# Kernel optimization log

Measured on AMD Instinct MI355X. Metric: run time of the kernel, lower is better.

The kernel has to match this reference:

```python
import jax, jax.numpy as jnp
import numpy as np
from jax import lax

SEQ, F, H1, H2, B, WV, OBJ, REL, VOCAB = 33, 20480, 900, 900, 2, 100, 35, 82, 117


def setup_inputs() -> dict:
    key = jax.random.key(0)
    ks = jax.random.split(key, 17)
    s = lambda k, shape: jax.random.normal(k, shape, jnp.float32) * 0.02
    return dict(
        x=jax.random.normal(ks[0], (SEQ, B, F), jnp.float32),
        w_ih1=s(ks[1], (4 * H1, F)), w_hh1=s(ks[2], (4 * H1, H1)),
        b_ih1=s(ks[3], (4 * H1,)), b_hh1=s(ks[4], (4 * H1,)),
        w_ih2=s(ks[5], (SEQ, 4 * H2, H1 + WV)), w_hh2=s(ks[6], (SEQ, 4 * H2, H2)),
        b_ih2=s(ks[7], (SEQ, 4 * H2)), b_hh2=s(ks[8], (SEQ, 4 * H2)),
        w_obj1=s(ks[9], (OBJ, H2)), b_obj1=s(ks[10], (OBJ,)),
        w_rel=s(ks[11], (REL, H2)), b_rel=s(ks[12], (REL,)),
        w_obj2=s(ks[13], (OBJ, H2)), b_obj2=s(ks[14], (OBJ,)),
        embed=s(ks[15], (VOCAB, WV)),
    )


def lstm_cell(xt, h, c, w_ih, w_hh, b_ih, b_hh):
    # torch gate order: input, forget, cell(g), output
    gates = xt @ w_ih.T + h @ w_hh.T + b_ih + b_hh
    i, f, g, o = jnp.split(gates, 4, axis=-1)
    c = jax.nn.sigmoid(f) * c + jax.nn.sigmoid(i) * jnp.tanh(g)
    h = jax.nn.sigmoid(o) * jnp.tanh(c)
    return h, c


def reference(x, w_ih1, w_hh1, b_ih1, b_hh1, w_ih2, w_hh2, b_ih2, b_hh2,
              w_obj1, b_obj1, w_rel, b_rel, w_obj2, b_obj2, embed):
    batch = x.shape[1]
    # layer-1 LSTM over full sequence
    def step1(carry, xt):
        h, c = lstm_cell(xt, carry[0], carry[1], w_ih1, w_hh1, b_ih1, b_hh1)
        return (h, c), h
    h0 = jnp.zeros((batch, H1), x.dtype)
    _, out1 = lax.scan(step1, (h0, h0), x)  # [SEQ, B, H1]

    # layer-2: first SEQ-2 cells with zero word vector, distinct weights per step
    wv0 = jnp.zeros((batch, WV), x.dtype)
    def step2(carry, inp):
        xt, wih, whh, bih, bhh = inp
        h, c = lstm_cell(jnp.concatenate([xt, wv0], axis=1), carry[0], carry[1], wih, whh, bih, bhh)
        return (h, c), None
    h20 = jnp.zeros((batch, H2), x.dtype)
    (h2, c2), _ = lax.scan(step2, (h20, h20),
                           (out1[:SEQ - 2], w_ih2[:SEQ - 2], w_hh2[:SEQ - 2],
                            b_ih2[:SEQ - 2], b_hh2[:SEQ - 2]))

    obj1 = h2 @ w_obj1.T + b_obj1                      # [B, 35]
    wv = embed[jnp.argmax(obj1, axis=1)]               # [B, 100]
    h2, c2 = lstm_cell(jnp.concatenate([out1[SEQ - 2], wv], axis=1), h2, c2,
                       w_ih2[SEQ - 2], w_hh2[SEQ - 2], b_ih2[SEQ - 2], b_hh2[SEQ - 2])

    rel = h2 @ w_rel.T + b_rel                         # [B, 82]
    wv = embed[jnp.argmax(rel, axis=1) + OBJ]
    h2, c2 = lstm_cell(jnp.concatenate([out1[SEQ - 1], wv], axis=1), h2, c2,
                       w_ih2[SEQ - 1], w_hh2[SEQ - 1], b_ih2[SEQ - 1], b_hh2[SEQ - 1])

    obj2 = h2 @ w_obj2.T + b_obj2                      # [B, 35]
    return (obj1, rel, obj2)
```

## Files before the change

kernel.cpp:

```cpp
#include <hip/hip_runtime.h>

#define SEQn 33
#define Fn   20480
#define Hn   900
#define Bn   2
#define WVn  100
#define OBJn 35
#define RELn 82
#define G4n  3600
#define Mn   66
#define NBLK 225

#define KS1  16
#define KSL1 (Fn/KS1)
#define RB1  25
#define RPB1 144
#define NC1  (KSL1/32)
#define WSTR 40
#define THR1 192

typedef __attribute__((ext_vector_type(8))) short bf16x8;
typedef __attribute__((ext_vector_type(4))) float f32x4;

__device__ __forceinline__ float sigf(float v){ return 1.f/(1.f+expf(-v)); }
__device__ __forceinline__ float dot4(float4 a, float4 b){ return a.x*b.x+a.y*b.y+a.z*b.z+a.w*b.w; }
__device__ __forceinline__ float wred(float v){
  #pragma unroll
  for (int d = 32; d >= 1; d >>= 1) v += __shfl_xor(v, d, 64);
  return v;
}
__device__ __forceinline__ float gload(const float* p){
  return __hip_atomic_load((const float*)p, __ATOMIC_RELAXED, __HIP_MEMORY_SCOPE_AGENT);
}
__device__ __forceinline__ void gstore(float* p, float v){
  __hip_atomic_store(p, v, __ATOMIC_RELAXED, __HIP_MEMORY_SCOPE_AGENT);
}
__device__ __forceinline__ unsigned short f2bf(float f){
  unsigned u = __float_as_uint(f);
  unsigned r = u + 0x7FFFu + ((u >> 16) & 1u);
  return (unsigned short)(r >> 16);
}
__device__ __forceinline__ float bf2f(unsigned short h){
  return __uint_as_float(((unsigned)h) << 16);
}

__device__ __forceinline__ void arrive_and_wait(unsigned* bar){
  unsigned g = __hip_atomic_load(&bar[0], __ATOMIC_RELAXED, __HIP_MEMORY_SCOPE_AGENT);
  const unsigned grp = (unsigned)blockIdx.x & 7u;
  const unsigned gsz = (grp == 0u) ? 29u : 28u;
  unsigned c = __hip_atomic_fetch_add(&bar[32 + grp*16], 1u, __ATOMIC_RELAXED, __HIP_MEMORY_SCOPE_AGENT);
  if (c == gsz - 1u) {
    unsigned c2 = __hip_atomic_fetch_add(&bar[16], 1u, __ATOMIC_RELAXED, __HIP_MEMORY_SCOPE_AGENT);
    if (c2 == 7u) {
      __hip_atomic_store(&bar[16], 0u, __ATOMIC_RELAXED, __HIP_MEMORY_SCOPE_AGENT);
      #pragma unroll
      for (int g8 = 0; g8 < 8; ++g8)
        __hip_atomic_store(&bar[32 + g8*16], 0u, __ATOMIC_RELAXED, __HIP_MEMORY_SCOPE_AGENT);
      asm volatile("s_waitcnt vmcnt(0)" ::: "memory");
      __hip_atomic_store(&bar[0], g + 1u, __ATOMIC_RELAXED, __HIP_MEMORY_SCOPE_AGENT);
      return;
    }
  }
  unsigned cur;
  do { __builtin_amdgcn_s_sleep(1);
       cur = __hip_atomic_load(&bar[0], __ATOMIC_RELAXED, __HIP_MEMORY_SCOPE_AGENT);
  } while (cur == g);
}

__device__ __forceinline__ void gbar(unsigned* bar){
  __syncthreads();
  if (threadIdx.x == 0) arrive_and_wait(bar);
  __syncthreads();
}

__device__ __forceinline__ void gbar_lite(unsigned* bar, int wv){
  asm volatile("" ::: "memory");
  if (wv == 0) asm volatile("s_waitcnt vmcnt(0)" ::: "memory");
  __builtin_amdgcn_sched_barrier(0);
  __builtin_amdgcn_s_barrier();
  __builtin_amdgcn_sched_barrier(0);
  if (threadIdx.x == 0) arrive_and_wait(bar);
  __builtin_amdgcn_sched_barrier(0);
  __builtin_amdgcn_s_barrier();
  __builtin_amdgcn_sched_barrier(0);
  asm volatile("" ::: "memory");
}

__global__ __launch_bounds__(THR1) void k1_mfma(
    const float* __restrict__ x, const float* __restrict__ w1,
    float* __restrict__ G1, unsigned* __restrict__ bar)
{
  const int tid = threadIdx.x;
  if (blockIdx.x == 0 && tid < 10) {
    if (tid == 0) __hip_atomic_store(&bar[0], 0u, __ATOMIC_RELAXED, __HIP_MEMORY_SCOPE_AGENT);
    else if (tid == 1) __hip_atomic_store(&bar[16], 0u, __ATOMIC_RELAXED, __HIP_MEMORY_SCOPE_AGENT);
    else __hip_atomic_store(&bar[32 + (tid-2)*16], 0u, __ATOMIC_RELAXED, __HIP_MEMORY_SCOPE_AGENT);
  }
  __shared__ unsigned short WhL[2][RPB1*WSTR], WlL[2][RPB1*WSTR];
  __shared__ unsigned short XhL[2][80*WSTR],  XlL[2][80*WSTR];

  const int rb = blockIdx.x % RB1;
  const int ks = blockIdx.x / RB1;
  const int r0 = rb * RPB1;
  const int kofs = ks * KSL1;
  const int wv_ = tid >> 6;
  const int lane = tid & 63;
  const int p = lane & 15;
  const int q = lane >> 4;

  f32x4 acc[3][5];
  #pragma unroll
  for (int rt = 0; rt < 3; ++rt)
    #pragma unroll
    for (int mt = 0; mt < 5; ++mt) acc[rt][mt] = (f32x4){0.f,0.f,0.f,0.f};

  float4 wr[6], xrg[4];

  #define ISSUE_STAGE(cc)                                                      \
    { const int kbase = kofs + (cc)*32;                                        \
      _Pragma("unroll")                                                        \
      for (int u = 0; u < 6; ++u) {                                            \
        const int idx = tid + u*THR1;                                          \
        const int row = idx >> 3, k4 = idx & 7;                                \
        wr[u] = *(const float4*)(w1 + (size_t)(r0+row)*Fn + kbase + k4*4);     \
      }                                                                        \
      _Pragma("unroll")                                                        \
      for (int u = 0; u < 4; ++u) {                                            \
        const int idx = tid + u*THR1;                                          \
        const int mrow = idx >> 3, k4 = idx & 7;                               \
        xrg[u] = (idx < 640 && mrow < Mn)                                      \
          ? *(const float4*)(x + (size_t)mrow*Fn + kbase + k4*4)               \
          : make_float4(0.f,0.f,0.f,0.f);                                      \
      }                                                                        \
    }

  #define CVTW(dsth, dstl, off, v)                                             \
    { const unsigned short h0=f2bf(v.x), h1=f2bf(v.y), h2=f2bf(v.z), h3=f2bf(v.w); \
      const unsigned short l0=f2bf(v.x-bf2f(h0)), l1=f2bf(v.y-bf2f(h1));       \
      const unsigned short l2=f2bf(v.z-bf2f(h2)), l3=f2bf(v.w-bf2f(h3));       \
      *(uint2*)&dsth[off] = make_uint2((unsigned)h0|((unsigned)h1<<16),        \
                                       (unsigned)h2|((unsigned)h3<<16));       \
      *(uint2*)&dstl[off] = make_uint2((unsigned)l0|((unsigned)l1<<16),        \
                                       (unsigned)l2|((unsigned)l3<<16));       \
    }

  #define WRITE_STAGE(bb)                                                     \
    { _Pragma("unroll")                                                       \
      for (int u = 0; u < 6; ++u) {                                           \
        const int idx = tid + u*THR1;                                         \
        const int row = idx >> 3, k4 = idx & 7;                               \
        CVTW(WhL[bb], WlL[bb], row*WSTR + k4*4, wr[u]);                       \
      }                                                                       \
      _Pragma("unroll")                                                       \
      for (int u = 0; u < 4; ++u) {                                           \
        const int idx = tid + u*THR1;                                         \
        if (idx < 640) {                                                      \
          const int mrow = idx >> 3, k4 = idx & 7;                            \
          CVTW(XhL[bb], XlL[bb], mrow*WSTR + k4*4, xrg[u]);                   \
        }                                                                     \
      }                                                                       \
    }

  ISSUE_STAGE(0);
  WRITE_STAGE(0);
  __syncthreads();

  for (int c = 0; c < NC1; ++c) {
    const int buf = c & 1;
    if (c+1 < NC1) ISSUE_STAGE(c+1);

    bf16x8 Bh[5], Bl[5];
    #pragma unroll
    for (int mt = 0; mt < 5; ++mt) {
      const int moff = (mt*16 + p)*WSTR + q*8;
      Bh[mt] = *(const bf16x8*)&XhL[buf][moff];
      Bl[mt] = *(const bf16x8*)&XlL[buf][moff];
    }
    #pragma unroll
    for (int rt = 0; rt < 3; ++rt) {
      const int roff = ((wv_ + 3*rt)*16 + p)*WSTR + q*8;
      const bf16x8 Ah = *(const bf16x8*)&WhL[buf][roff];
      const bf16x8 Al = *(const bf16x8*)&WlL[buf][roff];
      #pragma unroll
      for (int mt = 0; mt < 5; ++mt) {
        acc[rt][mt] = __builtin_amdgcn_mfma_f32_16x16x32_bf16(Ah, Bh[mt], acc[rt][mt], 0, 0, 0);
        acc[rt][mt] = __builtin_amdgcn_mfma_f32_16x16x32_bf16(Ah, Bl[mt], acc[rt][mt], 0, 0, 0);
        acc[rt][mt] = __builtin_amdgcn_mfma_f32_16x16x32_bf16(Al, Bh[mt], acc[rt][mt], 0, 0, 0);
      }
    }

    if (c+1 < NC1) WRITE_STAGE(buf^1);
    __syncthreads();
  }

  #pragma unroll
  for (int rt = 0; rt < 3; ++rt)
    #pragma unroll
    for (int mt = 0; mt < 5; ++mt) {
      const int m = mt*16 + p;
      if (m < Mn) {
        #pragma unroll
        for (int r4 = 0; r4 < 4; ++r4) {
          const int grow = r0 + (wv_ + 3*rt)*16 + q*4 + r4;
          atomicAdd(&G1[(size_t)grow*Mn + m], acc[rt][mt][r4]);
        }
      }
    }
  #undef ISSUE_STAGE
  #undef WRITE_STAGE
  #undef CVTW
}

__global__ __launch_bounds__(512) void k_rec(
    const float* __restrict__ G1, float* __restrict__ out1, float* __restrict__ h2arr,
    const float* __restrict__ whh1,
    const float* __restrict__ wih2, const float* __restrict__ whh2,
    const float* __restrict__ bih2, const float* __restrict__ bhh2,
    const float* __restrict__ bih1, const float* __restrict__ bhh1,
    const float* __restrict__ wobj1, const float* __restrict__ bobj1,
    const float* __restrict__ wrel,  const float* __restrict__ brel,
    const float* __restrict__ wobj2, const float* __restrict__ bobj2,
    const float* __restrict__ embed, float* __restrict__ dout,
    unsigned* __restrict__ bar)
{
  __shared__ float hls[Bn][904];
  __shared__ float h2l[Bn][904];
  __shared__ float wvls[Bn][104];
  __shared__ float gls[16][68];
  __shared__ float bls[SEQn][16];
  __shared__ float gexA[16][Bn], gexB[16][Bn];
  __shared__ float cA[4][Bn], cB[4][Bn];
  __shared__ float red[4];
  __shared__ int idxls[Bn];

  const int tid = threadIdx.x;
  const int blk = blockIdx.x;
  const int j0 = blk * 4;
  const int wv_ = tid >> 6;
  const int lane = tid & 63;

  if (tid < 8) {
    const int jj = tid >> 1, m = tid & 1;
    cA[jj][m] = 0.f; cB[jj][m] = 0.f;
    gstore(h2arr + ((size_t)0*Bn + m)*Hn + j0 + jj, 0.f);
  }

  for (int qq = tid; qq < 16*Mn; qq += 512) {
    const int rho = qq / Mn, t = qq % Mn;
    const int gate = rho >> 2, jj = rho & 3;
    const size_t rA = (size_t)gate*Hn + j0 + jj;
    gls[rho][t] = G1[rA*Mn + t] + bih1[rA] + bhh1[rA];
  }
  for (int qq = tid; qq < SEQn*16; qq += 512) {
    const int s = qq / 16, rho = qq % 16;
    const int gate = rho >> 2, jj = rho & 3;
    const size_t ro = (size_t)s*G4n + (size_t)gate*Hn + j0 + jj;
    bls[s][rho] = bih2[ro] + bhh2[ro];
  }

  float4 wAreg[2][4];
  #pragma unroll
  for (int ri = 0; ri < 2; ++ri) {
    const int rho = wv_*2 + ri;
    const int gate = rho >> 2, jj = rho & 3;
    const size_t row = (size_t)gate*Hn + j0 + jj;
    #pragma unroll
    for (int e = 0; e < 4; ++e) {
      const int k = lane*4 + e*256;
      wAreg[ri][e] = (k <= Hn-4) ? *(const float4*)(whh1 + row*Hn + k)
                                 : make_float4(0.f,0.f,0.f,0.f);
    }
  }

  float4 wiR[2][4], whR[2][4];
  #define ISSUE_W(sp, KMX)                                                   \
    { _Pragma("unroll")                                                      \
      for (int ri = 0; ri < 2; ++ri) {                                       \
        const int rho = wv_*2 + ri;                                          \
        const int gate = rho >> 2, jj = rho & 3;                             \
        const size_t ro = (size_t)(sp)*G4n + (size_t)gate*Hn + j0 + jj;      \
        const float* wI = wih2 + ro*1000;                                    \
        const float* wH = whh2 + ro*Hn;                                      \
        _Pragma("unroll")                                                    \
        for (int e = 0; e < 4; ++e) {                                        \
          const int k = lane*4 + e*256;                                      \
          if (k <= (KMX)) wiR[ri][e] = *(const float4*)(wI + k);             \
          if (k <= 896)   whR[ri][e] = *(const float4*)(wH + k);             \
        }                                                                    \
      }                                                                      \
    }

  #define UPD_A(ivar)                                                        \
    { const float cc = sigf(gexA[4+jj][m])*cA[jj][m]                         \
                     + sigf(gexA[jj][m])*tanhf(gexA[8+jj][m]);               \
      cA[jj][m] = cc;                                                        \
      gstore(out1 + ((size_t)(ivar)*Bn + m)*Hn + j0 + jj,                    \
             sigf(gexA[12+jj][m])*tanhf(cc)); }

  #define UPD_B(svar)                                                        \
    { const float cc = sigf(gexB[4+jj][m])*cB[jj][m]                         \
                     + sigf(gexB[jj][m])*tanhf(gexB[8+jj][m]);               \
      cB[jj][m] = cc;                                                        \
      gstore(h2arr + ((size_t)((svar)+1)*Bn + m)*Hn + j0 + jj,               \
             sigf(gexB[12+jj][m])*tanhf(cc)); }

  ISSUE_W(0, 896);
  __syncthreads();

  if (lane == 0) {
    #pragma unroll
    for (int ri = 0; ri < 2; ++ri) {
      const int rho = wv_*2 + ri;
      gexA[rho][0] = gls[rho][0];
      gexA[rho][1] = gls[rho][1];
    }
  }
  __syncthreads();
  if (tid < 8) { const int jj = tid >> 1, m = tid & 1; UPD_A(0); }
  gbar(bar);

  for (int iv = 1; iv <= 31; ++iv) {
    const int s = iv - 1;
    float4 hv[2][4], h2v[2][4];
    #pragma unroll
    for (int e = 0; e < 4; ++e) {
      const int k = lane*4 + e*256;
      #pragma unroll
      for (int m = 0; m < 2; ++m) {
        hv[m][e]  = (k <= 896) ? *(const float4*)(out1  + ((size_t)s*Bn + m)*Hn + k)
                               : make_float4(0.f,0.f,0.f,0.f);
        h2v[m][e] = (k <= 896) ? *(const float4*)(h2arr + ((size_t)s*Bn + m)*Hn + k)
                               : make_float4(0.f,0.f,0.f,0.f);
      }
    }
    #pragma unroll
    for (int ri = 0; ri < 2; ++ri) {
      const int rho = wv_*2 + ri;
      float a0=0.f, a1=0.f, b0=0.f, b1=0.f;
      #pragma unroll
      for (int e = 0; e < 4; ++e) {
        const int k = lane*4 + e*256;
        if (k <= 896) {
          a0 += dot4(wAreg[ri][e], hv[0][e]);  a1 += dot4(wAreg[ri][e], hv[1][e]);
          b0 += dot4(wiR[ri][e],   hv[0][e]);  b1 += dot4(wiR[ri][e],   hv[1][e]);
          b0 += dot4(whR[ri][e],  h2v[0][e]);  b1 += dot4(whR[ri][e],  h2v[1][e]);
        }
      }
      a0 = wred(a0); a1 = wred(a1); b0 = wred(b0); b1 = wred(b1);
      if (lane == 0) {
        gexA[rho][0] = a0 + gls[rho][iv*Bn + 0];
        gexA[rho][1] = a1 + gls[rho][iv*Bn + 1];
        const float bb = bls[s][rho];
        gexB[rho][0] = b0 + bb;
        gexB[rho][1] = b1 + bb;
      }
    }
    asm volatile("s_waitcnt lgkmcnt(0)" ::: "memory");
    __builtin_amdgcn_sched_barrier(0);
    ISSUE_W(iv, (iv >= 31) ? 996 : 896);
    __builtin_amdgcn_sched_barrier(0);
    __builtin_amdgcn_s_barrier();
    __builtin_amdgcn_sched_barrier(0);
    if (tid < 8) {
      const int jj = tid >> 1, m = tid & 1;
      UPD_A(iv);
      UPD_B(s);
    }
    gbar_lite(bar, wv_);
  }

  for (int i = 32; i < 37; ++i) {
    if (i == 33 || i == 35) {
      if (wv_ < 2) {
        const int m = wv_;
        const int nout = (i == 33) ? OBJn : RELn;
        const int off = (i == 33) ? 0 : Bn*OBJn;
        float v = -1e30f; int idx = 0;
        for (int o = lane; o < nout; o += 64) {
          float t = gload(dout + off + m*nout + o);
          if (t > v) { v = t; idx = o; }
        }
        #pragma unroll
        for (int d = 32; d >= 1; d >>= 1) {
          float ov = __shfl_xor(v, d, 64);
          int   oi = __shfl_xor(idx, d, 64);
          if (ov > v || (ov == v && oi < idx)) { v = ov; idx = oi; }
        }
        if (lane == 0) idxls[m] = idx + ((i == 35) ? OBJn : 0);
      }
      __syncthreads();
      for (int qq = tid; qq < Bn*104; qq += 512) {
        const int m = qq / 104, v4 = qq % 104;
        wvls[m][v4] = (v4 < WVn) ? embed[(size_t)idxls[m]*WVn + v4] : 0.f;
      }
      __syncthreads();
    }

    const bool hasA = (i == 32);
    const int  s = (i == 33) ? 31 : (i == 35) ? 32 : -1;
    const bool hasB = (s >= 0);
    const int  srcA = (i == 35) ? 32 : i-1;

    if (hasA || i == 35) {
      for (int qq = tid; qq < 1808; qq += 512) {
        const int m = qq / 904, kk = qq % 904;
        hls[m][kk] = (kk < 900)
          ? gload(out1 + ((size_t)srcA*Bn + m)*Hn + kk) : 0.f;
      }
    }
    if (hasB) {
      for (int qq = tid; qq < 1808; qq += 512) {
        const int m = qq / 904, kk = qq % 904;
        h2l[m][kk] = (kk < 900)
          ? gload(h2arr + ((size_t)s*Bn + m)*Hn + kk) : 0.f;
      }
    }
    __syncthreads();

    if (hasA) {
      #pragma unroll
      for (int ri = 0; ri < 2; ++ri) {
        const int rho = wv_*2 + ri;
        float a0 = 0.f, a1 = 0.f;
        #pragma unroll
        for (int e = 0; e < 4; ++e) {
          const int k = lane*4 + e*256;
          if (k <= Hn-4) {
            a0 += dot4(wAreg[ri][e], *(const float4*)&hls[0][k]);
            a1 += dot4(wAreg[ri][e], *(const float4*)&hls[1][k]);
          }
        }
        a0 = wred(a0); a1 = wred(a1);
        if (lane == 0) {
          gexA[rho][0] = a0 + gls[rho][32*Bn + 0];
          gexA[rho][1] = a1 + gls[rho][32*Bn + 1];
        }
      }
    }

    if (hasB) {
      #pragma unroll
      for (int ri = 0; ri < 2; ++ri) {
        const int rho = wv_*2 + ri;
        float b0 = 0.f, b1 = 0.f;
        #pragma unroll
        for (int e = 0; e < 4; ++e) {
          const int k = lane*4 + e*256;
          if (k <= 896) {
            b0 += dot4(wiR[ri][e], *(const float4*)&hls[0][k]);
            b1 += dot4(wiR[ri][e], *(const float4*)&hls[1][k]);
            b0 += dot4(whR[ri][e], *(const float4*)&h2l[0][k]);
            b1 += dot4(whR[ri][e], *(const float4*)&h2l[1][k]);
          } else if (k >= 900 && k <= 996) {
            b0 += dot4(wiR[ri][e], *(const float4*)&wvls[0][k-900]);
            b1 += dot4(wiR[ri][e], *(const float4*)&wvls[1][k-900]);
          }
        }
        b0 = wred(b0); b1 = wred(b1);
        if (lane == 0) {
          const float bb = bls[s][rho];
          gexB[rho][0] = b0 + bb;
          gexB[rho][1] = b1 + bb;
        }
      }
      if (i == 33) ISSUE_W(32, 996);
    }

    if (i == 32 || i == 34 || i == 36) {
      const int nout = (i == 34) ? RELn : OBJn;
      const float* wh  = (i == 32) ? wobj1 : (i == 34) ? wrel : wobj2;
      const float* bh_ = (i == 32) ? bobj1 : (i == 34) ? brel : bobj2;
      const int off = (i == 32) ? 0 : (i == 34) ? (Bn*OBJn) : (Bn*OBJn + Bn*RELn);
      const int hb = (i == 32) ? 31 : (i == 34) ? 32 : 33;
      if (blk < nout*Bn) {
        const int o = blk >> 1, m = blk & 1;
        float p = 0.f;
        if (tid < 225) {
          const float4 wv4 = *(const float4*)(wh + (size_t)o*Hn + tid*4);
          const float* hp = h2arr + ((size_t)hb*Bn + m)*Hn + tid*4;
          p = wv4.x*gload(hp+0) + wv4.y*gload(hp+1)
            + wv4.z*gload(hp+2) + wv4.w*gload(hp+3);
        }
        if (wv_ < 4) {
          const float pr = wred(p);
          if (lane == 0) red[wv_] = pr;
        }
        __syncthreads();
        if (tid == 0)
          gstore(&dout[off + m*nout + o], red[0]+red[1]+red[2]+red[3] + bh_[o]);
      }
    }

    __syncthreads();
    if (tid < 8) {
      const int jj = tid >> 1, m = tid & 1;
      if (hasA) UPD_A(32);
      if (i == 33) UPD_B(31);
      if (i == 35) UPD_B(32);
    }

    if (i < 36) gbar(bar);
  }
  #undef ISSUE_W
  #undef UPD_A
  #undef UPD_B
}

extern "C" void kernel_launch(void* const* d_in, const int* in_sizes, int n_in,
                              void* d_out, int out_size, void* d_ws, size_t ws_size,
                              hipStream_t stream)
{
  (void)in_sizes; (void)n_in; (void)out_size; (void)ws_size;
  const float* x     = (const float*)d_in[0];
  const float* wih1  = (const float*)d_in[1];
  const float* whh1  = (const float*)d_in[2];
  const float* bih1  = (const float*)d_in[3];
  const float* bhh1  = (const float*)d_in[4];
  const float* wih2  = (const float*)d_in[5];
  const float* whh2  = (const float*)d_in[6];
  const float* bih2  = (const float*)d_in[7];
  const float* bhh2  = (const float*)d_in[8];
  const float* wobj1 = (const float*)d_in[9];
  const float* bobj1 = (const float*)d_in[10];
  const float* wrel  = (const float*)d_in[11];
  const float* brel  = (const float*)d_in[12];
  const float* wobj2 = (const float*)d_in[13];
  const float* bobj2 = (const float*)d_in[14];
  const float* embed = (const float*)d_in[15];
  float* dout = (float*)d_out;

  float* ws = (float*)d_ws;
  float* G1    = ws;
  float* out1  = G1 + (size_t)G4n*Mn;
  float* h2arr = out1 + (size_t)SEQn*Bn*Hn;
  unsigned* bar = (unsigned*)(h2arr + (size_t)34*Bn*Hn);

  hipMemsetAsync(G1, 0, (size_t)G4n*Mn*sizeof(float), stream);
  hipLaunchKernelGGL(k1_mfma, dim3(RB1*KS1), dim3(THR1), 0, stream, x, wih1, G1, bar);

  void* args[19];
  args[0]  = (void*)&G1;    args[1]  = (void*)&out1;  args[2]  = (void*)&h2arr;
  args[3]  = (void*)&whh1;  args[4]  = (void*)&wih2;  args[5]  = (void*)&whh2;
  args[6]  = (void*)&bih2;  args[7]  = (void*)&bhh2;  args[8]  = (void*)&bih1;
  args[9]  = (void*)&bhh1;  args[10] = (void*)&wobj1; args[11] = (void*)&bobj1;
  args[12] = (void*)&wrel;  args[13] = (void*)&brel;  args[14] = (void*)&wobj2;
  args[15] = (void*)&bobj2; args[16] = (void*)&embed; args[17] = (void*)&dout;
  args[18] = (void*)&bar;
  hipLaunchCooperativeKernel((void*)k_rec, dim3(NBLK), dim3(512), args, 0, stream);
}
```

Measured before the change: 475.7 us.

## Split recurrent kernel over twice the blocks and double-buffer per-step weight prefetch

The recurrent cooperative kernel now runs 450 blocks of 256 threads, each owning 2 hidden units instead of 4. The grid barrier is widened to 16 arrival groups to match. Layer-2 step weights are kept in two register buffers, so the next step's weights are loaded before the current step's dot products rather than after. This aims to hide weight-load latency and spread the per-step work across more CUs. The kernel is also launched with an ordinary launch instead of a cooperative one, which relies on all 450 blocks being co-resident and adds barrier arrivals and register pressure.

```diff
diff --git a/kernel.cpp b/kernel.cpp
--- a/kernel.cpp
+++ b/kernel.cpp
@@ -9,7 +9,7 @@
 #define RELn 82
 #define G4n  3600
 #define Mn   66
-#define NBLK 225
+#define NBLK 450
 
 #define KS1  16
 #define KSL1 (Fn/KS1)
@@ -46,16 +46,16 @@
 
 __device__ __forceinline__ void arrive_and_wait(unsigned* bar){
   unsigned g = __hip_atomic_load(&bar[0], __ATOMIC_RELAXED, __HIP_MEMORY_SCOPE_AGENT);
-  const unsigned grp = (unsigned)blockIdx.x & 7u;
-  const unsigned gsz = (grp == 0u) ? 29u : 28u;
+  const unsigned grp = (unsigned)blockIdx.x & 15u;
+  const unsigned gsz = (grp < 2u) ? 29u : 28u;
   unsigned c = __hip_atomic_fetch_add(&bar[32 + grp*16], 1u, __ATOMIC_RELAXED, __HIP_MEMORY_SCOPE_AGENT);
   if (c == gsz - 1u) {
     unsigned c2 = __hip_atomic_fetch_add(&bar[16], 1u, __ATOMIC_RELAXED, __HIP_MEMORY_SCOPE_AGENT);
-    if (c2 == 7u) {
+    if (c2 == 15u) {
       __hip_atomic_store(&bar[16], 0u, __ATOMIC_RELAXED, __HIP_MEMORY_SCOPE_AGENT);
       #pragma unroll
-      for (int g8 = 0; g8 < 8; ++g8)
-        __hip_atomic_store(&bar[32 + g8*16], 0u, __ATOMIC_RELAXED, __HIP_MEMORY_SCOPE_AGENT);
+      for (int g16 = 0; g16 < 16; ++g16)
+        __hip_atomic_store(&bar[32 + g16*16], 0u, __ATOMIC_RELAXED, __HIP_MEMORY_SCOPE_AGENT);
       asm volatile("s_waitcnt vmcnt(0)" ::: "memory");
       __hip_atomic_store(&bar[0], g + 1u, __ATOMIC_RELAXED, __HIP_MEMORY_SCOPE_AGENT);
       return;
@@ -91,7 +91,7 @@
     float* __restrict__ G1, unsigned* __restrict__ bar)
 {
   const int tid = threadIdx.x;
-  if (blockIdx.x == 0 && tid < 10) {
+  if (blockIdx.x == 0 && tid < 18) {
     if (tid == 0) __hip_atomic_store(&bar[0], 0u, __ATOMIC_RELAXED, __HIP_MEMORY_SCOPE_AGENT);
     else if (tid == 1) __hip_atomic_store(&bar[16], 0u, __ATOMIC_RELAXED, __HIP_MEMORY_SCOPE_AGENT);
     else __hip_atomic_store(&bar[32 + (tid-2)*16], 0u, __ATOMIC_RELAXED, __HIP_MEMORY_SCOPE_AGENT);
@@ -211,7 +211,7 @@
   #undef CVTW
 }
 
-__global__ __launch_bounds__(512) void k_rec(
+__global__ __launch_bounds__(256, 2) void k_rec(
     const float* __restrict__ G1, float* __restrict__ out1, float* __restrict__ h2arr,
     const float* __restrict__ whh1,
     const float* __restrict__ wih2, const float* __restrict__ whh2,
@@ -226,34 +226,34 @@
   __shared__ float hls[Bn][904];
   __shared__ float h2l[Bn][904];
   __shared__ float wvls[Bn][104];
-  __shared__ float gls[16][68];
-  __shared__ float bls[SEQn][16];
-  __shared__ float gexA[16][Bn], gexB[16][Bn];
-  __shared__ float cA[4][Bn], cB[4][Bn];
+  __shared__ float gls[8][68];
+  __shared__ float bls[SEQn][8];
+  __shared__ float gexA[8][Bn], gexB[8][Bn];
+  __shared__ float cA[2][Bn], cB[2][Bn];
   __shared__ float red[4];
   __shared__ int idxls[Bn];
 
   const int tid = threadIdx.x;
   const int blk = blockIdx.x;
-  const int j0 = blk * 4;
+  const int j0 = blk * 2;
   const int wv_ = tid >> 6;
   const int lane = tid & 63;
 
-  if (tid < 8) {
+  if (tid < 4) {
     const int jj = tid >> 1, m = tid & 1;
     cA[jj][m] = 0.f; cB[jj][m] = 0.f;
     gstore(h2arr + ((size_t)0*Bn + m)*Hn + j0 + jj, 0.f);
   }
 
-  for (int qq = tid; qq < 16*Mn; qq += 512) {
+  for (int qq = tid; qq < 8*Mn; qq += 256) {
     const int rho = qq / Mn, t = qq % Mn;
-    const int gate = rho >> 2, jj = rho & 3;
+    const int gate = rho >> 1, jj = rho & 1;
     const size_t rA = (size_t)gate*Hn + j0 + jj;
     gls[rho][t] = G1[rA*Mn + t] + bih1[rA] + bhh1[rA];
   }
-  for (int qq = tid; qq < SEQn*16; qq += 512) {
-    const int s = qq / 16, rho = qq % 16;
-    const int gate = rho >> 2, jj = rho & 3;
+  for (int qq = tid; qq < SEQn*8; qq += 256) {
+    const int s = qq / 8, rho = qq % 8;
+    const int gate = rho >> 1, jj = rho & 1;
     const size_t ro = (size_t)s*G4n + (size_t)gate*Hn + j0 + jj;
     bls[s][rho] = bih2[ro] + bhh2[ro];
   }
@@ -262,7 +262,7 @@
   #pragma unroll
   for (int ri = 0; ri < 2; ++ri) {
     const int rho = wv_*2 + ri;
-    const int gate = rho >> 2, jj = rho & 3;
+    const int gate = rho >> 1, jj = rho & 1;
     const size_t row = (size_t)gate*Hn + j0 + jj;
     #pragma unroll
     for (int e = 0; e < 4; ++e) {
@@ -272,39 +272,89 @@
     }
   }
 
-  float4 wiR[2][4], whR[2][4];
-  #define ISSUE_W(sp, KMX)                                                   \
+  float4 wiR0[2][4], whR0[2][4], wiR1[2][4], whR1[2][4];
+  #define ISSUE_W(sp, WI, WH, KMX)                                           \
     { _Pragma("unroll")                                                      \
       for (int ri = 0; ri < 2; ++ri) {                                       \
         const int rho = wv_*2 + ri;                                          \
-        const int gate = rho >> 2, jj = rho & 3;                             \
+        const int gate = rho >> 1, jj = rho & 1;                             \
         const size_t ro = (size_t)(sp)*G4n + (size_t)gate*Hn + j0 + jj;      \
         const float* wI = wih2 + ro*1000;                                    \
         const float* wH = whh2 + ro*Hn;                                      \
         _Pragma("unroll")                                                    \
         for (int e = 0; e < 4; ++e) {                                        \
           const int k = lane*4 + e*256;                                      \
-          if (k <= (KMX)) wiR[ri][e] = *(const float4*)(wI + k);             \
-          if (k <= 896)   whR[ri][e] = *(const float4*)(wH + k);             \
+          if (k <= (KMX)) WI[ri][e] = *(const float4*)(wI + k);              \
+          if (k <= 896)   WH[ri][e] = *(const float4*)(wH + k);              \
         }                                                                    \
       }                                                                      \
     }
 
   #define UPD_A(ivar)                                                        \
-    { const float cc = sigf(gexA[4+jj][m])*cA[jj][m]                         \
-                     + sigf(gexA[jj][m])*tanhf(gexA[8+jj][m]);               \
+    { const float cc = sigf(gexA[2+jj][m])*cA[jj][m]                         \
+                     + sigf(gexA[jj][m])*tanhf(gexA[4+jj][m]);               \
       cA[jj][m] = cc;                                                        \
       gstore(out1 + ((size_t)(ivar)*Bn + m)*Hn + j0 + jj,                    \
-             sigf(gexA[12+jj][m])*tanhf(cc)); }
+             sigf(gexA[6+jj][m])*tanhf(cc)); }
 
   #define UPD_B(svar)                                                        \
-    { const float cc = sigf(gexB[4+jj][m])*cB[jj][m]                         \
-                     + sigf(gexB[jj][m])*tanhf(gexB[8+jj][m]);               \
+    { const float cc = sigf(gexB[2+jj][m])*cB[jj][m]                         \
+                     + sigf(gexB[jj][m])*tanhf(gexB[4+jj][m]);               \
       cB[jj][m] = cc;                                                        \
       gstore(h2arr + ((size_t)((svar)+1)*Bn + m)*Hn + j0 + jj,               \
-             sigf(gexB[12+jj][m])*tanhf(cc)); }
-
-  ISSUE_W(0, 896);
+             sigf(gexB[6+jj][m])*tanhf(cc)); }
+
+  #define STEP(iv, WIu, WHu, WIa, WHa)                                       \
+    { const int s = (iv) - 1;                                                \
+      float4 hv[2][4], h2v[2][4];                                            \
+      _Pragma("unroll")                                                      \
+      for (int e = 0; e < 4; ++e) {                                          \
+        const int k = lane*4 + e*256;                                        \
+        _Pragma("unroll")                                                    \
+        for (int m = 0; m < 2; ++m) {                                        \
+          hv[m][e]  = (k <= 896) ? *(const float4*)(out1  + ((size_t)s*Bn + m)*Hn + k)  \
+                                 : make_float4(0.f,0.f,0.f,0.f);             \
+          h2v[m][e] = (k <= 896) ? *(const float4*)(h2arr + ((size_t)s*Bn + m)*Hn + k)  \
+                                 : make_float4(0.f,0.f,0.f,0.f);             \
+        }                                                                    \
+      }                                                                      \
+      __builtin_amdgcn_sched_barrier(0);                                     \
+      ISSUE_W((iv), WIa, WHa, ((iv) >= 31) ? 996 : 896);                     \
+      __builtin_amdgcn_sched_barrier(0);                                     \
+      _Pragma("unroll")                                                      \
+      for (int ri = 0; ri < 2; ++ri) {                                       \
+        const int rho = wv_*2 + ri;                                          \
+        float a0=0.f, a1=0.f, b0=0.f, b1=0.f;                                \
+        _Pragma("unroll")                                                    \
+        for (int e = 0; e < 4; ++e) {                                        \
+          const int k = lane*4 + e*256;                                      \
+          if (k <= 896) {                                                    \
+            a0 += dot4(wAreg[ri][e], hv[0][e]);  a1 += dot4(wAreg[ri][e], hv[1][e]);   \
+            b0 += dot4(WIu[ri][e],   hv[0][e]);  b1 += dot4(WIu[ri][e],   hv[1][e]);   \
+            b0 += dot4(WHu[ri][e],  h2v[0][e]);  b1 += dot4(WHu[ri][e],  h2v[1][e]);   \
+          }                                                                  \
+        }                                                                    \
+        a0 = wred(a0); a1 = wred(a1); b0 = wred(b0); b1 = wred(b1);          \
+        if (lane == 0) {                                                     \
+          gexA[rho][0] = a0 + gls[rho][(iv)*Bn + 0];                         \
+          gexA[rho][1] = a1 + gls[rho][(iv)*Bn + 1];                         \
+          const float bb = bls[s][rho];                                      \
+          gexB[rho][0] = b0 + bb;                                            \
+          gexB[rho][1] = b1 + bb;                                            \
+        }                                                                    \
+      }                                                                      \
+      asm volatile("s_waitcnt lgkmcnt(0)" ::: "memory");                     \
+      __builtin_amdgcn_sched_barrier(0);                                     \
+      __builtin_amdgcn_s_barrier();                                          \
+      __builtin_amdgcn_sched_barrier(0);                                     \
+      if (tid < 4) {                                                         \
+        const int jj = tid >> 1, m = tid & 1;                                \
+        UPD_A(iv);                                                           \
+        UPD_B(s);                                                            \
+      }                                                                      \
+      gbar_lite(bar, wv_); }
+
+  ISSUE_W(0, wiR0, whR0, 896);
   __syncthreads();
 
   if (lane == 0) {
@@ -316,58 +366,14 @@
     }
   }
   __syncthreads();
-  if (tid < 8) { const int jj = tid >> 1, m = tid & 1; UPD_A(0); }
+  if (tid < 4) { const int jj = tid >> 1, m = tid & 1; UPD_A(0); }
   gbar(bar);
 
-  for (int iv = 1; iv <= 31; ++iv) {
-    const int s = iv - 1;
-    float4 hv[2][4], h2v[2][4];
-    #pragma unroll
-    for (int e = 0; e < 4; ++e) {
-      const int k = lane*4 + e*256;
-      #pragma unroll
-      for (int m = 0; m < 2; ++m) {
-        hv[m][e]  = (k <= 896) ? *(const float4*)(out1  + ((size_t)s*Bn + m)*Hn + k)
-                               : make_float4(0.f,0.f,0.f,0.f);
-        h2v[m][e] = (k <= 896) ? *(const float4*)(h2arr + ((size_t)s*Bn + m)*Hn + k)
-                               : make_float4(0.f,0.f,0.f,0.f);
-      }
-    }
-    #pragma unroll
-    for (int ri = 0; ri < 2; ++ri) {
-      const int rho = wv_*2 + ri;
-      float a0=0.f, a1=0.f, b0=0.f, b1=0.f;
-      #pragma unroll
-      for (int e = 0; e < 4; ++e) {
-        const int k = lane*4 + e*256;
-        if (k <= 896) {
-          a0 += dot4(wAreg[ri][e], hv[0][e]);  a1 += dot4(wAreg[ri][e], hv[1][e]);
-          b0 += dot4(wiR[ri][e],   hv[0][e]);  b1 += dot4(wiR[ri][e],   hv[1][e]);
-          b0 += dot4(whR[ri][e],  h2v[0][e]);  b1 += dot4(whR[ri][e],  h2v[1][e]);
-        }
-      }
-      a0 = wred(a0); a1 = wred(a1); b0 = wred(b0); b1 = wred(b1);
-      if (lane == 0) {
-        gexA[rho][0] = a0 + gls[rho][iv*Bn + 0];
-        gexA[rho][1] = a1 + gls[rho][iv*Bn + 1];
-        const float bb = bls[s][rho];
-        gexB[rho][0] = b0 + bb;
-        gexB[rho][1] = b1 + bb;
-      }
-    }
-    asm volatile("s_waitcnt lgkmcnt(0)" ::: "memory");
-    __builtin_amdgcn_sched_barrier(0);
-    ISSUE_W(iv, (iv >= 31) ? 996 : 896);
-    __builtin_amdgcn_sched_barrier(0);
-    __builtin_amdgcn_s_barrier();
-    __builtin_amdgcn_sched_barrier(0);
-    if (tid < 8) {
-      const int jj = tid >> 1, m = tid & 1;
-      UPD_A(iv);
-      UPD_B(s);
-    }
-    gbar_lite(bar, wv_);
-  }
+  for (int ib = 1; ib <= 29; ib += 2) {
+    STEP(ib,   wiR0, whR0, wiR1, whR1);
+    STEP(ib+1, wiR1, whR1, wiR0, whR0);
+  }
+  STEP(31, wiR0, whR0, wiR1, whR1);
 
   for (int i = 32; i < 37; ++i) {
     if (i == 33 || i == 35) {
@@ -389,7 +395,7 @@
         if (lane == 0) idxls[m] = idx + ((i == 35) ? OBJn : 0);
       }
       __syncthreads();
-      for (int qq = tid; qq < Bn*104; qq += 512) {
+      for (int qq = tid; qq < Bn*104; qq += 256) {
         const int m = qq / 104, v4 = qq % 104;
         wvls[m][v4] = (v4 < WVn) ? embed[(size_t)idxls[m]*WVn + v4] : 0.f;
       }
@@ -402,14 +408,14 @@
     const int  srcA = (i == 35) ? 32 : i-1;
 
     if (hasA || i == 35) {
-      for (int qq = tid; qq < 1808; qq += 512) {
+      for (int qq = tid; qq < 1808; qq += 256) {
         const int m = qq / 904, kk = qq % 904;
         hls[m][kk] = (kk < 900)
           ? gload(out1 + ((size_t)srcA*Bn + m)*Hn + kk) : 0.f;
       }
     }
     if (hasB) {
-      for (int qq = tid; qq < 1808; qq += 512) {
+      for (int qq = tid; qq < 1808; qq += 256) {
         const int m = qq / 904, kk = qq % 904;
         h2l[m][kk] = (kk < 900)
           ? gload(h2arr + ((size_t)s*Bn + m)*Hn + kk) : 0.f;
@@ -447,13 +453,25 @@
         for (int e = 0; e < 4; ++e) {
           const int k = lane*4 + e*256;
           if (k <= 896) {
-            b0 += dot4(wiR[ri][e], *(const float4*)&hls[0][k]);
-            b1 += dot4(wiR[ri][e], *(const float4*)&hls[1][k]);
-            b0 += dot4(whR[ri][e], *(const float4*)&h2l[0][k]);
-            b1 += dot4(whR[ri][e], *(const float4*)&h2l[1][k]);
+            if (i == 33) {
+              b0 += dot4(wiR1[ri][e], *(const float4*)&hls[0][k]);
+              b1 += dot4(wiR1[ri][e], *(const float4*)&hls[1][k]);
+              b0 += dot4(whR1[ri][e], *(const float4*)&h2l[0][k]);
+              b1 += dot4(whR1[ri][e], *(const float4*)&h2l[1][k]);
+            } else {
+              b0 += dot4(wiR0[ri][e], *(const float4*)&hls[0][k]);
+              b1 += dot4(wiR0[ri][e], *(const float4*)&hls[1][k]);
+              b0 += dot4(whR0[ri][e], *(const float4*)&h2l[0][k]);
+              b1 += dot4(whR0[ri][e], *(const float4*)&h2l[1][k]);
+            }
           } else if (k >= 900 && k <= 996) {
-            b0 += dot4(wiR[ri][e], *(const float4*)&wvls[0][k-900]);
-            b1 += dot4(wiR[ri][e], *(const float4*)&wvls[1][k-900]);
+            if (i == 33) {
+              b0 += dot4(wiR1[ri][e], *(const float4*)&wvls[0][k-900]);
+              b1 += dot4(wiR1[ri][e], *(const float4*)&wvls[1][k-900]);
+            } else {
+              b0 += dot4(wiR0[ri][e], *(const float4*)&wvls[0][k-900]);
+              b1 += dot4(wiR0[ri][e], *(const float4*)&wvls[1][k-900]);
+            }
           }
         }
         b0 = wred(b0); b1 = wred(b1);
@@ -463,7 +481,7 @@
           gexB[rho][1] = b1 + bb;
         }
       }
-      if (i == 33) ISSUE_W(32, 996);
+      if (i == 33) ISSUE_W(32, wiR0, whR0, 996);
     }
 
     if (i == 32 || i == 34 || i == 36) {
@@ -481,10 +499,8 @@
           p = wv4.x*gload(hp+0) + wv4.y*gload(hp+1)
             + wv4.z*gload(hp+2) + wv4.w*gload(hp+3);
         }
-        if (wv_ < 4) {
-          const float pr = wred(p);
-          if (lane == 0) red[wv_] = pr;
-        }
+        const float pr = wred(p);
+        if (lane == 0) red[wv_] = pr;
         __syncthreads();
         if (tid == 0)
           gstore(&dout[off + m*nout + o], red[0]+red[1]+red[2]+red[3] + bh_[o]);
@@ -492,7 +508,7 @@
     }
 
     __syncthreads();
-    if (tid < 8) {
+    if (tid < 4) {
       const int jj = tid >> 1, m = tid & 1;
       if (hasA) UPD_A(32);
       if (i == 33) UPD_B(31);
@@ -504,6 +520,7 @@
   #undef ISSUE_W
   #undef UPD_A
   #undef UPD_B
+  #undef STEP
 }
 
 extern "C" void kernel_launch(void* const* d_in, const int* in_sizes, int n_in,
@@ -537,14 +554,7 @@
 
   hipMemsetAsync(G1, 0, (size_t)G4n*Mn*sizeof(float), stream);
   hipLaunchKernelGGL(k1_mfma, dim3(RB1*KS1), dim3(THR1), 0, stream, x, wih1, G1, bar);
-
-  void* args[19];
-  args[0]  = (void*)&G1;    args[1]  = (void*)&out1;  args[2]  = (void*)&h2arr;
-  args[3]  = (void*)&whh1;  args[4]  = (void*)&wih2;  args[5]  = (void*)&whh2;
-  args[6]  = (void*)&bih2;  args[7]  = (void*)&bhh2;  args[8]  = (void*)&bih1;
-  args[9]  = (void*)&bhh1;  args[10] = (void*)&wobj1; args[11] = (void*)&bobj1;
-  args[12] = (void*)&wrel;  args[13] = (void*)&brel;  args[14] = (void*)&wobj2;
-  args[15] = (void*)&bobj2; args[16] = (void*)&embed; args[17] = (void*)&dout;
-  args[18] = (void*)&bar;
-  hipLaunchCooperativeKernel((void*)k_rec, dim3(NBLK), dim3(512), args, 0, stream);
-}
+  hipLaunchKernelGGL(k_rec, dim3(NBLK), dim3(256), 0, stream,
+                     G1, out1, h2arr, whh1, wih2, whh2, bih2, bhh2, bih1, bhh1,
+                     wobj1, bobj1, wrel, brel, wobj2, bobj2, embed, dout, bar);
+}
```

After: 688.6 us. 44.8% more time.
